# Performance work log

Measured on AMD Instinct MI355X. Metric: run time of the kernel, lower is better.

Reference implementation:

```python
import jax, jax.numpy as jnp
import numpy as np

N, E = 50000, 800000
F_NODE, F_EDGE, H, LAT, MAXN = 128, 16, 128, 64, 200


def setup_inputs() -> dict:
    key = jax.random.key(0)
    ks = jax.random.split(key, 40)
    s = 0.05
    p = {
        'x': jax.random.normal(ks[0], (N, F_NODE), jnp.float32),
        'edge_index': jax.random.randint(ks[1], (2, E), 0, N, jnp.int64),
        'edge_attr': jax.random.normal(ks[2], (E, F_EDGE), jnp.float32),
        'eps': jax.random.normal(ks[3], (1, LAT), jnp.float32),
        'num_nodes': N,
        # GATConv layer 1 (heads=1)
        'W1': jax.random.normal(ks[4], (F_NODE, H), jnp.float32) * s,
        'att_src1': jax.random.normal(ks[5], (H,), jnp.float32) * s,
        'att_dst1': jax.random.normal(ks[6], (H,), jnp.float32) * s,
        'We1': jax.random.normal(ks[7], (F_EDGE, H), jnp.float32) * s,
        'att_e1': jax.random.normal(ks[8], (H,), jnp.float32) * s,
        'b1': jnp.zeros((H,), jnp.float32),
        # GATConv layer 2
        'W2': jax.random.normal(ks[9], (H, H), jnp.float32) * s,
        'att_src2': jax.random.normal(ks[10], (H,), jnp.float32) * s,
        'att_dst2': jax.random.normal(ks[11], (H,), jnp.float32) * s,
        'We2': jax.random.normal(ks[12], (F_EDGE, H), jnp.float32) * s,
        'att_e2': jax.random.normal(ks[13], (H,), jnp.float32) * s,
        'b2': jnp.zeros((H,), jnp.float32),
        # heads
        'mu_W': jax.random.normal(ks[14], (H, LAT), jnp.float32) * s,
        'mu_b': jnp.zeros((LAT,), jnp.float32),
        'lv_W': jax.random.normal(ks[15], (H, LAT), jnp.float32) * s,
        'lv_b': jnp.zeros((LAT,), jnp.float32),
        'dec_W': jax.random.normal(ks[16], (LAT, H), jnp.float32) * s,
        'dec_b': jnp.zeros((H,), jnp.float32),
        'adj_W1': jax.random.normal(ks[17], (H, H), jnp.float32) * s,
        'adj_b1': jnp.zeros((H,), jnp.float32),
        'adj_W2': jax.random.normal(ks[18], (H, MAXN), jnp.float32) * s,
        'adj_b2': jnp.zeros((MAXN,), jnp.float32),
        'nd_W1': jax.random.normal(ks[19], (H, H), jnp.float32) * s,
        'nd_b1': jnp.zeros((H,), jnp.float32),
        'nd_W2': jax.random.normal(ks[20], (H, F_NODE), jnp.float32) * s,
        'nd_b2': jnp.zeros((F_NODE,), jnp.float32),
    }
    return p


def _gat(h, src, dst, ea, W, a_s, a_d, We, a_e, b, n):
    # PyG GATConv, heads=1: linear transform, per-edge attention, segment softmax over dst
    g = h @ W                                     # [n, H]
    alpha = jax.nn.leaky_relu((g @ a_s)[src] + (g @ a_d)[dst] + (ea @ We) @ a_e,
                              negative_slope=0.2)  # [E']
    m = jax.ops.segment_max(alpha, dst, num_segments=n)
    ex = jnp.exp(alpha - m[dst])
    den = jax.ops.segment_sum(ex, dst, num_segments=n)
    w = ex / den[dst]
    return jax.ops.segment_sum(w[:, None] * g[src], dst, num_segments=n) + b


def _forward(x, edge_index, edge_attr, eps, num_nodes,
             W1, att_src1, att_dst1, We1, att_e1, b1,
             W2, att_src2, att_dst2, We2, att_e2, b2,
             mu_W, mu_b, lv_W, lv_b, dec_W, dec_b,
             adj_W1, adj_b1, adj_W2, adj_b2, nd_W1, nd_b1, nd_W2, nd_b2):
    n = x.shape[0]
    src, dst = edge_index[0], edge_index[1]
    # add self loops; self-loop edge_attr = per-node mean of incoming edge_attr (PyG fill_value='mean')
    deg = jax.ops.segment_sum(jnp.ones((src.shape[0],), x.dtype), dst, num_segments=n)
    mean_ea = jax.ops.segment_sum(edge_attr, dst, num_segments=n) / jnp.maximum(deg, 1.0)[:, None]
    loop = jnp.arange(n)
    src_f = jnp.concatenate([src, loop])
    dst_f = jnp.concatenate([dst, loop])
    ea_f = jnp.concatenate([edge_attr, mean_ea])
    h = jax.nn.relu(_gat(x, src_f, dst_f, ea_f, W1, att_src1, att_dst1, We1, att_e1, b1, n))
    h = jax.nn.relu(_gat(h, src_f, dst_f, ea_f, W2, att_src2, att_dst2, We2, att_e2, b2, n))
    hg = h.mean(axis=0, keepdims=True)            # global_mean_pool, single graph -> [1, H]
    mu = hg @ mu_W + mu_b
    logvar = hg @ lv_W + lv_b
    z = mu + eps * jnp.exp(0.5 * logvar)
    hd = jax.nn.relu(z @ dec_W + dec_b)           # [1, H]
    hn = jnp.broadcast_to(hd[:, None, :], (1, num_nodes, hd.shape[-1]))
    adj = jax.nn.relu(hn @ adj_W1 + adj_b1) @ adj_W2 + adj_b2   # [1, n, MAXN]
    adj = adj[:, :, :num_nodes]
    nodes = jax.nn.relu(hn @ nd_W1 + nd_b1) @ nd_W2 + nd_b2     # [1, n, F_NODE]
    return adj, nodes, mu, logvar


def reference(x, edge_index, edge_attr, eps, num_nodes,
              W1, att_src1, att_dst1, We1, att_e1, b1,
              W2, att_src2, att_dst2, We2, att_e2, b2,
              mu_W, mu_b, lv_W, lv_b, dec_W, dec_b,
              adj_W1, adj_b1, adj_W2, adj_b2, nd_W1, nd_b1, nd_W2, nd_b2):
    return _forward(x, edge_index, edge_attr, eps, num_nodes,
                    W1, att_src1, att_dst1, We1, att_e1, b1,
                    W2, att_src2, att_dst2, We2, att_e2, b2,
                    mu_W, mu_b, lv_W, lv_b, dec_W, dec_b,
                    adj_W1, adj_b1, adj_W2, adj_b2, nd_W1, nd_b1, nd_W2, nd_b2)
```

## Files before the change

### kernel.cpp

```cpp
#include <hip/hip_runtime.h>
#include <math.h>

#define NN   50000
#define EE   800000
#define EF   850000
#define HH   128
#define FE   16
#define LATD 64
#define MAXNN 200

#define ADJ_TOT   10000000
#define NODES_TOT 6400000
#define OUT_TOT   16400000
#define MU_OFF    16400000
#define LV_OFF    16400064

__device__ __forceinline__ unsigned short f2bf(float f){
  unsigned int u = __float_as_uint(f);
  unsigned int r = (u + 0x7FFFu + ((u>>16)&1u)) >> 16;
  return (unsigned short)r;
}
__device__ __forceinline__ float bf2f(unsigned short h){
  return __uint_as_float(((unsigned int)h)<<16);
}

__global__ void kinit(int* ideg, float* hgsum){
  int i = blockIdx.x*blockDim.x + threadIdx.x;
  if(i < NN) ideg[i]=0;
  if(i < HH) hgsum[i]=0.f;
}

__global__ void kwa(const float* We1, const float* ae1, const float* We2, const float* ae2,
                    float* wa1, float* wa2){
  int t = threadIdx.x;
  if(t < FE){
    float s1=0.f, s2=0.f;
    for(int j=0;j<HH;j++){ s1 += We1[t*HH+j]*ae1[j]; s2 += We2[t*HH+j]*ae2[j]; }
    wa1[t]=s1; wa2[t]=s2;
  }
}

__global__ void kdeg(const int* __restrict__ ei, int* ideg, int* __restrict__ erank){
  int e = blockIdx.x*blockDim.x + threadIdx.x;
  if(e<EE) erank[e] = atomicAdd(&ideg[ei[EE+e]], 1);
}

__global__ void kscan1(const int* __restrict__ ideg, int* rowstart, int* blocksum){
  __shared__ int sd[1024];
  int t=threadIdx.x; int i=blockIdx.x*1024+t;
  int v = (i<NN)? (ideg[i]+1) : 0;
  sd[t]=v; __syncthreads();
  for(int off=1; off<1024; off<<=1){
    int x = (t>=off)? sd[t-off] : 0;
    __syncthreads();
    sd[t] += x;
    __syncthreads();
  }
  if(i<NN) rowstart[i] = sd[t]-v;
  if(t==1023) blocksum[blockIdx.x]=sd[1023];
}
__global__ void kscan2(const int* blocksum, int* blockoff, int nb){
  if(threadIdx.x==0){
    int run=0;
    for(int b=0;b<nb;b++){ blockoff[b]=run; run+=blocksum[b]; }
    blockoff[nb]=run;
  }
}
__global__ void kscan3(int* rowstart, const int* __restrict__ blockoff, int nb){
  int i=blockIdx.x*blockDim.x+threadIdx.x;
  if(i<NN) rowstart[i]+=blockoff[i>>10];
  if(i==0) rowstart[NN]=blockoff[nb];
}

__global__ void kscatter(const int* __restrict__ ei, const float* __restrict__ ea,
                         const float* __restrict__ wa1, const float* __restrict__ wa2,
                         const int* __restrict__ rowstart, const int* __restrict__ erank,
                         float4* __restrict__ csr){
  int e=blockIdx.x*blockDim.x+threadIdx.x;
  if(e>=EE) return;
  int s=ei[e], d=ei[EE+e];
  const float4* ea4 = (const float4*)(ea + (size_t)e*FE);
  float4 v0=ea4[0], v1=ea4[1], v2=ea4[2], v3=ea4[3];
  float va[16]={v0.x,v0.y,v0.z,v0.w, v1.x,v1.y,v1.z,v1.w,
                v2.x,v2.y,v2.z,v2.w, v3.x,v3.y,v3.z,v3.w};
  float d1=0.f,d2=0.f;
  #pragma unroll
  for(int f=0;f<FE;f++){ d1+=va[f]*wa1[f]; d2+=va[f]*wa2[f]; }
  int pos = rowstart[d] + erank[e];
  csr[pos] = make_float4(__int_as_float(s), d1, d2, 0.f);
}

__global__ __launch_bounds__(256) void kself(const int* __restrict__ rowstart,
                      const int* __restrict__ ideg,
                      float4* __restrict__ csr){
  int tid = threadIdx.x;
  int l16 = tid & 15;
  int grp = tid >> 4;
  int i = blockIdx.x*16 + grp;
  if(i>=NN) return;
  int base = rowstart[i]; int deg = ideg[i];
  float s1=0.f, s2=0.f;
  for(int k=l16;k<deg;k+=16){ float4 en=csr[base+k]; s1+=en.y; s2+=en.z; }
  #pragma unroll
  for(int m=8;m>=1;m>>=1){ s1+=__shfl_xor(s1,m,16); s2+=__shfl_xor(s2,m,16); }
  if(l16==0){
    float dg = (float)deg; if(dg<1.f) dg=1.f;
    csr[base+deg] = make_float4(__int_as_float(i), s1/dg, s2/dg, 0.f);
  }
}

__global__ __launch_bounds__(256) void kgemm2(const float* __restrict__ hin,
    const float* __restrict__ W,
    const float* __restrict__ atts, const float* __restrict__ attd,
    unsigned short* __restrict__ Gbf, float* __restrict__ asrc, float* __restrict__ adst){
  __shared__ float hs[64*HH];
  int t = threadIdx.x;
  int row0 = blockIdx.x * 64;
  #pragma unroll
  for(int it=0; it<8; ++it){
    int f = it*256 + t;
    int r = f >> 5;
    int c4 = f & 31;
    int grow = row0 + r;
    float4 v = make_float4(0.f,0.f,0.f,0.f);
    if(grow < NN) v = *(const float4*)(hin + (size_t)grow*HH + c4*4);
    int sc4 = c4 ^ ((r>>3)&3);
    *(float4*)(hs + r*HH + sc4*4) = v;
  }
  __syncthreads();

  int tcg = t & 15;
  int trg = t >> 4;
  int c0  = tcg*8;
  int r0  = trg*4;
  int sw  = (trg>>1)&3;

  float s_att[8], d_att[8];
  #pragma unroll
  for(int c=0;c<8;c++){ s_att[c]=atts[c0+c]; d_att[c]=attd[c0+c]; }

  float acc[4][8];
  #pragma unroll
  for(int r=0;r<4;r++)
    #pragma unroll
    for(int c=0;c<8;c++) acc[r][c]=0.f;

  for(int k=0;k<HH;k+=4){
    int k4 = k>>2;
    float4 hv[4];
    #pragma unroll
    for(int r=0;r<4;r++)
      hv[r] = *(const float4*)(hs + (r0+r)*HH + ((k4 ^ sw)<<2));
    #pragma unroll
    for(int kk=0;kk<4;kk++){
      float4 w0 = *(const float4*)(W + (size_t)(k+kk)*HH + c0);
      float4 w1 = *(const float4*)(W + (size_t)(k+kk)*HH + c0 + 4);
      float wz[8] = {w0.x,w0.y,w0.z,w0.w,w1.x,w1.y,w1.z,w1.w};
      #pragma unroll
      for(int r=0;r<4;r++){
        float hval = (kk==0)?hv[r].x : (kk==1)?hv[r].y : (kk==2)?hv[r].z : hv[r].w;
        #pragma unroll
        for(int c=0;c<8;c++) acc[r][c] += hval * wz[c];
      }
    }
  }

  #pragma unroll
  for(int r=0;r<4;r++){
    int grow = row0 + r0 + r;
    float ps=0.f, pd=0.f;
    #pragma unroll
    for(int c=0;c<8;c++){ ps += acc[r][c]*s_att[c]; pd += acc[r][c]*d_att[c]; }
    #pragma unroll
    for(int m=8;m>=1;m>>=1){ ps += __shfl_xor(ps,m,16); pd += __shfl_xor(pd,m,16); }
    if(grow < NN){
      uint4 o;
      o.x = (unsigned)f2bf(acc[r][0]) | ((unsigned)f2bf(acc[r][1])<<16);
      o.y = (unsigned)f2bf(acc[r][2]) | ((unsigned)f2bf(acc[r][3])<<16);
      o.z = (unsigned)f2bf(acc[r][4]) | ((unsigned)f2bf(acc[r][5])<<16);
      o.w = (unsigned)f2bf(acc[r][6]) | ((unsigned)f2bf(acc[r][7])<<16);
      *(uint4*)(Gbf + (size_t)grow*HH + c0) = o;
      if(tcg==0){ asrc[grow]=ps; adst[grow]=pd; }
    }
  }
}

__global__ __launch_bounds__(256) void kgat(const unsigned short* __restrict__ A,
    const float* __restrict__ asrc, const float* __restrict__ adst,
    const int* __restrict__ rowstart, const float4* __restrict__ csr,
    int etsel, const float* __restrict__ bias,
    float* __restrict__ alphabuf, int* __restrict__ srcbuf,
    float* __restrict__ Bout){
  int lane = threadIdx.x & 63;
  int wid  = threadIdx.x >> 6;
  int i = blockIdx.x*4 + wid;
  if(i >= NN) return;
  int base = rowstart[i]; int len = rowstart[i+1]-base;
  float adi = adst[i];
  float acc0=0.f, acc1=0.f;
  float den;
  if(__builtin_expect(len <= 64, 1)){
    float a = -1e30f; int s=0;
    if(lane < len){
      float4 en = csr[base+lane];
      s = __float_as_int(en.x);
      float et = etsel ? en.z : en.y;
      a = asrc[s] + adi + et;
      a = a>0.f ? a : 0.2f*a;
    }
    float m = a;
    #pragma unroll
    for(int mk=32;mk>=1;mk>>=1) m = fmaxf(m, __shfl_xor(m, mk));
    float ex = (lane<len) ? __expf(a-m) : 0.f;
    float sm = ex;
    #pragma unroll
    for(int mk=32;mk>=1;mk>>=1) sm += __shfl_xor(sm, mk);
    den = sm;
    const unsigned short* Ap = A + lane*2;
    int k=0;
    for(; k+4<=len; k+=4){
      float wk0=__shfl(ex,k+0); int sk0=__shfl(s,k+0);
      float wk1=__shfl(ex,k+1); int sk1=__shfl(s,k+1);
      float wk2=__shfl(ex,k+2); int sk2=__shfl(s,k+2);
      float wk3=__shfl(ex,k+3); int sk3=__shfl(s,k+3);
      unsigned p0 = *(const unsigned*)(Ap + (size_t)sk0*HH);
      unsigned p1 = *(const unsigned*)(Ap + (size_t)sk1*HH);
      unsigned p2 = *(const unsigned*)(Ap + (size_t)sk2*HH);
      unsigned p3 = *(const unsigned*)(Ap + (size_t)sk3*HH);
      acc0 += wk0 * __uint_as_float(p0<<16);
      acc1 += wk0 * __uint_as_float(p0 & 0xFFFF0000u);
      acc0 += wk1 * __uint_as_float(p1<<16);
      acc1 += wk1 * __uint_as_float(p1 & 0xFFFF0000u);
      acc0 += wk2 * __uint_as_float(p2<<16);
      acc1 += wk2 * __uint_as_float(p2 & 0xFFFF0000u);
      acc0 += wk3 * __uint_as_float(p3<<16);
      acc1 += wk3 * __uint_as_float(p3 & 0xFFFF0000u);
    }
    for(; k<len; k++){
      float wk = __shfl(ex, k);
      int   sk = __shfl(s, k);
      unsigned pr = *(const unsigned*)(Ap + (size_t)sk*HH);
      acc0 += wk * __uint_as_float(pr<<16);
      acc1 += wk * __uint_as_float(pr & 0xFFFF0000u);
    }
  } else {
    float lm = -1e30f;
    for(int k=lane;k<len;k+=64){
      float4 en = csr[base+k];
      int s = __float_as_int(en.x);
      float et = etsel ? en.z : en.y;
      float a = asrc[s] + adi + et;
      a = a>0.f ? a : 0.2f*a;
      alphabuf[base+k]=a; srcbuf[base+k]=s;
      lm = fmaxf(lm,a);
    }
    #pragma unroll
    for(int mk=32;mk>=1;mk>>=1) lm = fmaxf(lm, __shfl_xor(lm, mk));
    float ls=0.f;
    for(int k=lane;k<len;k+=64){
      float ex = __expf(alphabuf[base+k]-lm);
      alphabuf[base+k]=ex; ls+=ex;
    }
    #pragma unroll
    for(int mk=32;mk>=1;mk>>=1) ls += __shfl_xor(ls, mk);
    den = ls;
    for(int c=0;c<len;c+=64){
      int kk = c+lane;
      float w = (kk<len)? alphabuf[base+kk] : 0.f;
      int   s = (kk<len)? srcbuf[base+kk] : 0;
      int lim = min(64, len-c);
      for(int j=0;j<lim;j++){
        float wk = __shfl(w, j);
        int   sk = __shfl(s, j);
        unsigned pr = *(const unsigned*)(A + (size_t)sk*HH + lane*2);
        acc0 += wk * __uint_as_float(pr<<16);
        acc1 += wk * __uint_as_float(pr & 0xFFFF0000u);
      }
    }
  }
  float inv = 1.f/den;
  float2 bb = *(const float2*)(bias + lane*2);
  float2 o;
  o.x = fmaxf(acc0*inv + bb.x, 0.f);
  o.y = fmaxf(acc1*inv + bb.y, 0.f);
  *(float2*)(Bout + (size_t)i*HH + lane*2) = o;
}

__global__ __launch_bounds__(256) void khg(const float* __restrict__ B, float* hgsum){
  int f = threadIdx.x & 127;
  int half = threadIdx.x >> 7;
  float s=0.f;
  for(int i = blockIdx.x*2+half; i < NN; i += gridDim.x*2)
    s += B[(size_t)i*HH + f];
  __shared__ float sd[256];
  sd[threadIdx.x]=s; __syncthreads();
  if(half==0) atomicAdd(&hgsum[f], sd[threadIdx.x]+sd[threadIdx.x+128]);
}

__global__ __launch_bounds__(256) void kdec(const float* __restrict__ hgsum, const float* __restrict__ eps,
   const float* muW,const float* mub,const float* lvW,const float* lvb,
   const float* decW,const float* decb,
   const float* aW1,const float* ab1,const float* aW2,const float* ab2,
   const float* nW1,const float* nb1,const float* nW2,const float* nb2,
   float* out, float* rowadj, float* rownodes){
  __shared__ float hg[HH], z[LATD], hd[HH], t1[HH], t2[HH];
  int t=threadIdx.x;
  if(t<HH) hg[t]=hgsum[t]*(1.0f/NN);
  __syncthreads();
  if(t<LATD){
    float mu=mub[t], lv=lvb[t];
    for(int k=0;k<HH;k++){ mu += hg[k]*muW[k*LATD+t]; lv += hg[k]*lvW[k*LATD+t]; }
    out[MU_OFF+t]=mu; out[LV_OFF+t]=lv;
    z[t]=mu + eps[t]*expf(0.5f*lv);
  }
  __syncthreads();
  if(t<HH){
    float a=decb[t];
    for(int k=0;k<LATD;k++) a += z[k]*decW[k*HH+t];
    hd[t]=fmaxf(a,0.f);
  }
  __syncthreads();
  if(t<HH){
    float a=ab1[t];
    for(int k=0;k<HH;k++) a += hd[k]*aW1[k*HH+t];
    t1[t]=fmaxf(a,0.f);
  } else {
    int j=t-HH;
    float a=nb1[j];
    for(int k=0;k<HH;k++) a += hd[k]*nW1[k*HH+j];
    t2[j]=fmaxf(a,0.f);
  }
  __syncthreads();
  for(int j=t;j<MAXNN;j+=256){
    float a=ab2[j];
    for(int k=0;k<HH;k++) a += t1[k]*aW2[k*MAXNN+j];
    rowadj[j]=a;
  }
  if(t<HH){
    float a=nb2[t];
    for(int k=0;k<HH;k++) a += t2[k]*nW2[k*HH+t];
    rownodes[t]=a;
  }
}

__global__ __launch_bounds__(256) void kbcast(const float* __restrict__ rowadj,
                                              const float* __restrict__ rownodes,
                                              float* __restrict__ out){
  __shared__ float row[MAXNN+HH];
  int t=threadIdx.x;
  if(t<MAXNN) row[t]=rowadj[t];
  if(t<HH) row[MAXNN+t]=rownodes[t];
  __syncthreads();
  int stride=gridDim.x*blockDim.x;
  for(int idx=blockIdx.x*blockDim.x+t; idx<OUT_TOT; idx+=stride){
    if(idx<ADJ_TOT) out[idx]=row[idx%MAXNN];
    else { int j=(idx-ADJ_TOT)&(HH-1); out[idx]=row[MAXNN+j]; }
  }
}

extern "C" void kernel_launch(void* const* d_in, const int* in_sizes, int n_in,
                              void* d_out, int out_size, void* d_ws, size_t ws_size,
                              hipStream_t stream){
  const float* x   = (const float*)d_in[0];
  const int*   ei  = (const int*)d_in[1];
  const float* ea  = (const float*)d_in[2];
  const float* eps = (const float*)d_in[3];
  const float* W1  =(const float*)d_in[5];
  const float* as1 =(const float*)d_in[6];
  const float* ad1 =(const float*)d_in[7];
  const float* We1 =(const float*)d_in[8];
  const float* ae1 =(const float*)d_in[9];
  const float* b1  =(const float*)d_in[10];
  const float* W2  =(const float*)d_in[11];
  const float* as2 =(const float*)d_in[12];
  const float* ad2 =(const float*)d_in[13];
  const float* We2 =(const float*)d_in[14];
  const float* ae2 =(const float*)d_in[15];
  const float* b2  =(const float*)d_in[16];
  const float* muW =(const float*)d_in[17];
  const float* mub =(const float*)d_in[18];
  const float* lvW =(const float*)d_in[19];
  const float* lvb =(const float*)d_in[20];
  const float* decW=(const float*)d_in[21];
  const float* decb=(const float*)d_in[22];
  const float* aW1 =(const float*)d_in[23];
  const float* ab1 =(const float*)d_in[24];
  const float* aW2 =(const float*)d_in[25];
  const float* ab2 =(const float*)d_in[26];
  const float* nW1 =(const float*)d_in[27];
  const float* nb1 =(const float*)d_in[28];
  const float* nW2 =(const float*)d_in[29];
  const float* nb2 =(const float*)d_in[30];
  float* out=(float*)d_out;

  char* w=(char*)d_ws;
  unsigned short* Abf = (unsigned short*)w; w += (size_t)NN*HH*2;
  float*  Bb       = (float*)w;  w += (size_t)NN*HH*4;
  float4* csr      = (float4*)w; w += (size_t)EF*16;
  float*  alphabuf = (float*)w;  w += (size_t)EF*4;
  int*    srcbuf   = (int*)w;    w += (size_t)EF*4;
  int*    erank    = (int*)w;    w += (size_t)EE*4;
  int*    rowstart = (int*)w;    w += (size_t)(NN+1)*4;
  int*    ideg     = (int*)w;    w += (size_t)NN*4;
  float*  asrc     = (float*)w;  w += (size_t)NN*4;
  float*  adst     = (float*)w;  w += (size_t)NN*4;
  float*  hgsum    = (float*)w;  w += 128*4;
  float*  wa1      = (float*)w;  w += 16*4;
  float*  wa2      = (float*)w;  w += 16*4;
  float*  rowadj   = (float*)w;  w += 256*4;
  float*  rownodes = (float*)w;  w += 128*4;
  int*    blocksum = (int*)w;    w += 64*4;
  int*    blockoff = (int*)w;    w += 64*4;

  int nb = (NN+1023)/1024;
  int gemmblocks = (NN+63)/64;
  int gatblocks  = (NN+3)/4;

  hipLaunchKernelGGL(kinit, dim3((NN+255)/256), dim3(256), 0, stream, ideg, hgsum);
  hipLaunchKernelGGL(kwa, dim3(1), dim3(64), 0, stream, We1, ae1, We2, ae2, wa1, wa2);
  hipLaunchKernelGGL(kdeg, dim3((EE+255)/256), dim3(256), 0, stream, ei, ideg, erank);
  hipLaunchKernelGGL(kscan1, dim3(nb), dim3(1024), 0, stream, ideg, rowstart, blocksum);
  hipLaunchKernelGGL(kscan2, dim3(1), dim3(64), 0, stream, blocksum, blockoff, nb);
  hipLaunchKernelGGL(kscan3, dim3((NN+255)/256), dim3(256), 0, stream, rowstart, blockoff, nb);
  hipLaunchKernelGGL(kscatter, dim3((EE+255)/256), dim3(256), 0, stream,
                     ei, ea, wa1, wa2, rowstart, erank, csr);
  hipLaunchKernelGGL(kself, dim3((NN+15)/16), dim3(256), 0, stream, rowstart, ideg, csr);
  hipLaunchKernelGGL(kgemm2, dim3(gemmblocks), dim3(256), 0, stream, x,  W1, as1, ad1, Abf, asrc, adst);
  hipLaunchKernelGGL(kgat,  dim3(gatblocks), dim3(256), 0, stream, Abf, asrc, adst, rowstart, csr, 0, b1, alphabuf, srcbuf, Bb);
  hipLaunchKernelGGL(kgemm2, dim3(gemmblocks), dim3(256), 0, stream, Bb, W2, as2, ad2, Abf, asrc, adst);
  hipLaunchKernelGGL(kgat,  dim3(gatblocks), dim3(256), 0, stream, Abf, asrc, adst, rowstart, csr, 1, b2, alphabuf, srcbuf, Bb);
  hipLaunchKernelGGL(khg,   dim3(512), dim3(256), 0, stream, Bb, hgsum);
  hipLaunchKernelGGL(kdec,  dim3(1), dim3(256), 0, stream, hgsum, eps,
                     muW,mub,lvW,lvb,decW,decb,aW1,ab1,aW2,ab2,nW1,nb1,nW2,nb2,
                     out, rowadj, rownodes);
  hipLaunchKernelGGL(kbcast, dim3(2048), dim3(256), 0, stream, rowadj, rownodes, out);
}
```

Baseline: 485.6 us.

## Use bf16 MFMA for node GEMMs and store layer outputs in bf16

Replaces the FP32 shared-memory register-tiled GEMM with a bf16 MFMA 16x16x32 kernel that reads the input rows directly and uses a pre-transposed bf16 weight matrix built by a new prep kernel. The GAT layer output buffer becomes bf16 instead of fp32, which halves its write traffic and the reads in the second GEMM and the mean-pool kernel. This trades precision in the intermediate activations for lower memory traffic and faster matrix math. The epilogue now writes 2-byte elements with scattered stores rather than 16-byte vectors.

```diff
diff --git a/kernel.cpp b/kernel.cpp
--- a/kernel.cpp
+++ b/kernel.cpp
@@ -15,6 +15,9 @@
 #define MU_OFF    16400000
 #define LV_OFF    16400064
 
+typedef __attribute__((ext_vector_type(8))) short bf16x8;
+typedef __attribute__((ext_vector_type(4))) float f32x4;
+
 __device__ __forceinline__ unsigned short f2bf(float f){
   unsigned int u = __float_as_uint(f);
   unsigned int r = (u + 0x7FFFu + ((u>>16)&1u)) >> 16;
@@ -37,6 +40,16 @@
     float s1=0.f, s2=0.f;
     for(int j=0;j<HH;j++){ s1 += We1[t*HH+j]*ae1[j]; s2 += We2[t*HH+j]*ae2[j]; }
     wa1[t]=s1; wa2[t]=s2;
+  }
+}
+
+__global__ void kwprep(const float* __restrict__ W1, const float* __restrict__ W2,
+                       unsigned short* __restrict__ Wp1, unsigned short* __restrict__ Wp2){
+  int t = blockIdx.x*256 + threadIdx.x;
+  if(t < HH*HH){
+    int n = t >> 7, k = t & 127;
+    Wp1[t] = f2bf(W1[k*HH + n]);
+    Wp2[t] = f2bf(W2[k*HH + n]);
   }
 }
 
@@ -109,80 +122,59 @@
   }
 }
 
-__global__ __launch_bounds__(256) void kgemm2(const float* __restrict__ hin,
-    const float* __restrict__ W,
+__global__ __launch_bounds__(256) void kgemm3(const void* __restrict__ hin, int h_is_fp32,
+    const unsigned short* __restrict__ Wp,
     const float* __restrict__ atts, const float* __restrict__ attd,
     unsigned short* __restrict__ Gbf, float* __restrict__ asrc, float* __restrict__ adst){
-  __shared__ float hs[64*HH];
-  int t = threadIdx.x;
-  int row0 = blockIdx.x * 64;
-  #pragma unroll
-  for(int it=0; it<8; ++it){
-    int f = it*256 + t;
-    int r = f >> 5;
-    int c4 = f & 31;
-    int grow = row0 + r;
-    float4 v = make_float4(0.f,0.f,0.f,0.f);
-    if(grow < NN) v = *(const float4*)(hin + (size_t)grow*HH + c4*4);
-    int sc4 = c4 ^ ((r>>3)&3);
-    *(float4*)(hs + r*HH + sc4*4) = v;
-  }
-  __syncthreads();
-
-  int tcg = t & 15;
-  int trg = t >> 4;
-  int c0  = tcg*8;
-  int r0  = trg*4;
-  int sw  = (trg>>1)&3;
-
-  float s_att[8], d_att[8];
-  #pragma unroll
-  for(int c=0;c<8;c++){ s_att[c]=atts[c0+c]; d_att[c]=attd[c0+c]; }
-
-  float acc[4][8];
-  #pragma unroll
-  for(int r=0;r<4;r++)
-    #pragma unroll
-    for(int c=0;c<8;c++) acc[r][c]=0.f;
-
-  for(int k=0;k<HH;k+=4){
-    int k4 = k>>2;
-    float4 hv[4];
-    #pragma unroll
-    for(int r=0;r<4;r++)
-      hv[r] = *(const float4*)(hs + (r0+r)*HH + ((k4 ^ sw)<<2));
-    #pragma unroll
-    for(int kk=0;kk<4;kk++){
-      float4 w0 = *(const float4*)(W + (size_t)(k+kk)*HH + c0);
-      float4 w1 = *(const float4*)(W + (size_t)(k+kk)*HH + c0 + 4);
-      float wz[8] = {w0.x,w0.y,w0.z,w0.w,w1.x,w1.y,w1.z,w1.w};
-      #pragma unroll
-      for(int r=0;r<4;r++){
-        float hval = (kk==0)?hv[r].x : (kk==1)?hv[r].y : (kk==2)?hv[r].z : hv[r].w;
-        #pragma unroll
-        for(int c=0;c<8;c++) acc[r][c] += hval * wz[c];
-      }
-    }
-  }
-
-  #pragma unroll
-  for(int r=0;r<4;r++){
-    int grow = row0 + r0 + r;
+  int lane = threadIdx.x & 63;
+  int wid  = threadIdx.x >> 6;
+  int l = lane & 15, q = lane >> 4;
+  int r0 = blockIdx.x*64 + wid*16;
+  if(r0 >= NN) return;
+  const unsigned short* hb = (const unsigned short*)hin;
+  const float*          hf = (const float*)hin;
+  int row = r0 + l;
+
+  f32x4 acc[8];
+  #pragma unroll
+  for(int t=0;t<8;t++) acc[t]=(f32x4){0.f,0.f,0.f,0.f};
+
+  #pragma unroll
+  for(int kb=0;kb<4;kb++){
+    bf16x8 a;
+    if(h_is_fp32){
+      const float* p = hf + (size_t)row*HH + kb*32 + q*8;
+      float4 u0 = *(const float4*)(p);
+      float4 u1 = *(const float4*)(p+4);
+      a[0]=(short)f2bf(u0.x); a[1]=(short)f2bf(u0.y); a[2]=(short)f2bf(u0.z); a[3]=(short)f2bf(u0.w);
+      a[4]=(short)f2bf(u1.x); a[5]=(short)f2bf(u1.y); a[6]=(short)f2bf(u1.z); a[7]=(short)f2bf(u1.w);
+    } else {
+      a = *(const bf16x8*)(hb + (size_t)row*HH + kb*32 + q*8);
+    }
+    #pragma unroll
+    for(int t=0;t<8;t++){
+      bf16x8 b = *(const bf16x8*)(Wp + (size_t)(t*16+l)*HH + kb*32 + q*8);
+      acc[t] = __builtin_amdgcn_mfma_f32_16x16x32_bf16(a, b, acc[t], 0,0,0);
+    }
+  }
+
+  float av[8], dv[8];
+  #pragma unroll
+  for(int t=0;t<8;t++){ av[t]=atts[t*16+l]; dv[t]=attd[t*16+l]; }
+  #pragma unroll
+  for(int reg=0;reg<4;reg++){
     float ps=0.f, pd=0.f;
     #pragma unroll
-    for(int c=0;c<8;c++){ ps += acc[r][c]*s_att[c]; pd += acc[r][c]*d_att[c]; }
-    #pragma unroll
-    for(int m=8;m>=1;m>>=1){ ps += __shfl_xor(ps,m,16); pd += __shfl_xor(pd,m,16); }
-    if(grow < NN){
-      uint4 o;
-      o.x = (unsigned)f2bf(acc[r][0]) | ((unsigned)f2bf(acc[r][1])<<16);
-      o.y = (unsigned)f2bf(acc[r][2]) | ((unsigned)f2bf(acc[r][3])<<16);
-      o.z = (unsigned)f2bf(acc[r][4]) | ((unsigned)f2bf(acc[r][5])<<16);
-      o.w = (unsigned)f2bf(acc[r][6]) | ((unsigned)f2bf(acc[r][7])<<16);
-      *(uint4*)(Gbf + (size_t)grow*HH + c0) = o;
-      if(tcg==0){ asrc[grow]=ps; adst[grow]=pd; }
-    }
-  }
+    for(int t=0;t<8;t++){ ps+=acc[t][reg]*av[t]; pd+=acc[t][reg]*dv[t]; }
+    #pragma unroll
+    for(int m=8;m>=1;m>>=1){ ps+=__shfl_xor(ps,m,16); pd+=__shfl_xor(pd,m,16); }
+    if(l==0){ int R=r0+q*4+reg; asrc[R]=ps; adst[R]=pd; }
+  }
+  #pragma unroll
+  for(int t=0;t<8;t++)
+    #pragma unroll
+    for(int reg=0;reg<4;reg++)
+      Gbf[(size_t)(r0+q*4+reg)*HH + t*16 + l] = f2bf(acc[t][reg]);
 }
 
 __global__ __launch_bounds__(256) void kgat(const unsigned short* __restrict__ A,
@@ -190,7 +182,7 @@
     const int* __restrict__ rowstart, const float4* __restrict__ csr,
     int etsel, const float* __restrict__ bias,
     float* __restrict__ alphabuf, int* __restrict__ srcbuf,
-    float* __restrict__ Bout){
+    unsigned short* __restrict__ Bout){
   int lane = threadIdx.x & 63;
   int wid  = threadIdx.x >> 6;
   int i = blockIdx.x*4 + wid;
@@ -280,18 +272,18 @@
   }
   float inv = 1.f/den;
   float2 bb = *(const float2*)(bias + lane*2);
-  float2 o;
-  o.x = fmaxf(acc0*inv + bb.x, 0.f);
-  o.y = fmaxf(acc1*inv + bb.y, 0.f);
-  *(float2*)(Bout + (size_t)i*HH + lane*2) = o;
-}
-
-__global__ __launch_bounds__(256) void khg(const float* __restrict__ B, float* hgsum){
+  float ox = fmaxf(acc0*inv + bb.x, 0.f);
+  float oy = fmaxf(acc1*inv + bb.y, 0.f);
+  unsigned ov = (unsigned)f2bf(ox) | ((unsigned)f2bf(oy)<<16);
+  *(unsigned*)(Bout + (size_t)i*HH + lane*2) = ov;
+}
+
+__global__ __launch_bounds__(256) void khg(const unsigned short* __restrict__ B, float* hgsum){
   int f = threadIdx.x & 127;
   int half = threadIdx.x >> 7;
   float s=0.f;
   for(int i = blockIdx.x*2+half; i < NN; i += gridDim.x*2)
-    s += B[(size_t)i*HH + f];
+    s += bf2f(B[(size_t)i*HH + f]);
   __shared__ float sd[256];
   sd[threadIdx.x]=s; __syncthreads();
   if(half==0) atomicAdd(&hgsum[f], sd[threadIdx.x]+sd[threadIdx.x+128]);
@@ -395,7 +387,9 @@
 
   char* w=(char*)d_ws;
   unsigned short* Abf = (unsigned short*)w; w += (size_t)NN*HH*2;
-  float*  Bb       = (float*)w;  w += (size_t)NN*HH*4;
+  unsigned short* Bbf = (unsigned short*)w; w += (size_t)NN*HH*2;
+  unsigned short* Wp1 = (unsigned short*)w; w += (size_t)HH*HH*2;
+  unsigned short* Wp2 = (unsigned short*)w; w += (size_t)HH*HH*2;
   float4* csr      = (float4*)w; w += (size_t)EF*16;
   float*  alphabuf = (float*)w;  w += (size_t)EF*4;
   int*    srcbuf   = (int*)w;    w += (size_t)EF*4;
@@ -418,6 +412,7 @@
 
   hipLaunchKernelGGL(kinit, dim3((NN+255)/256), dim3(256), 0, stream, ideg, hgsum);
   hipLaunchKernelGGL(kwa, dim3(1), dim3(64), 0, stream, We1, ae1, We2, ae2, wa1, wa2);
+  hipLaunchKernelGGL(kwprep, dim3((HH*HH+255)/256), dim3(256), 0, stream, W1, W2, Wp1, Wp2);
   hipLaunchKernelGGL(kdeg, dim3((EE+255)/256), dim3(256), 0, stream, ei, ideg, erank);
   hipLaunchKernelGGL(kscan1, dim3(nb), dim3(1024), 0, stream, ideg, rowstart, blocksum);
   hipLaunchKernelGGL(kscan2, dim3(1), dim3(64), 0, stream, blocksum, blockoff, nb);
@@ -425,11 +420,13 @@
   hipLaunchKernelGGL(kscatter, dim3((EE+255)/256), dim3(256), 0, stream,
                      ei, ea, wa1, wa2, rowstart, erank, csr);
   hipLaunchKernelGGL(kself, dim3((NN+15)/16), dim3(256), 0, stream, rowstart, ideg, csr);
-  hipLaunchKernelGGL(kgemm2, dim3(gemmblocks), dim3(256), 0, stream, x,  W1, as1, ad1, Abf, asrc, adst);
-  hipLaunchKernelGGL(kgat,  dim3(gatblocks), dim3(256), 0, stream, Abf, asrc, adst, rowstart, csr, 0, b1, alphabuf, srcbuf, Bb);
-  hipLaunchKernelGGL(kgemm2, dim3(gemmblocks), dim3(256), 0, stream, Bb, W2, as2, ad2, Abf, asrc, adst);
-  hipLaunchKernelGGL(kgat,  dim3(gatblocks), dim3(256), 0, stream, Abf, asrc, adst, rowstart, csr, 1, b2, alphabuf, srcbuf, Bb);
-  hipLaunchKernelGGL(khg,   dim3(512), dim3(256), 0, stream, Bb, hgsum);
+  hipLaunchKernelGGL(kgemm3, dim3(gemmblocks), dim3(256), 0, stream,
+                     (const void*)x, 1, Wp1, as1, ad1, Abf, asrc, adst);
+  hipLaunchKernelGGL(kgat,  dim3(gatblocks), dim3(256), 0, stream, Abf, asrc, adst, rowstart, csr, 0, b1, alphabuf, srcbuf, Bbf);
+  hipLaunchKernelGGL(kgemm3, dim3(gemmblocks), dim3(256), 0, stream,
+                     (const void*)Bbf, 0, Wp2, as2, ad2, Abf, asrc, adst);
+  hipLaunchKernelGGL(kgat,  dim3(gatblocks), dim3(256), 0, stream, Abf, asrc, adst, rowstart, csr, 1, b2, alphabuf, srcbuf, Bbf);
+  hipLaunchKernelGGL(khg,   dim3(512), dim3(256), 0, stream, Bbf, hgsum);
   hipLaunchKernelGGL(kdec,  dim3(1), dim3(256), 0, stream, hgsum, eps,
                      muW,mub,lvW,lvb,decW,decb,aW1,ab1,aW2,ab2,nW1,nb1,nW2,nb2,
                      out, rowadj, rownodes);
```

After: 453.5 us. -6.6%, faster.
